# Kernel tuning notes

Hardware: AMD Instinct MI355X
Metric: run time of the kernel (lower is better)

## Reference

```python
import jax, jax.numpy as jnp
import numpy as np

E = 1024      # embed_dim
H = 16        # num_heads
HD = E // H   # head_dim = 64
R = 8         # dora rank
T, B = 2048, 2


def setup_inputs() -> dict:
    key = jax.random.key(0)
    ks = jax.random.split(key, 16)
    query = jax.random.normal(ks[0], (T, B, E), dtype=jnp.float32)
    kk = jax.random.normal(ks[1], (T, B, E), dtype=jnp.float32)
    vv = jax.random.normal(ks[2], (T, B, E), dtype=jnp.float32)

    def make_dora(k1, k2, k3, k4):
        w = jax.random.normal(k1, (E, E), dtype=jnp.float32) * (E ** -0.5)
        m = jnp.linalg.norm(w)            # magnitude scalar (Frobenius norm)
        V = w / m                          # frozen direction, ||V||_F = 1
        A = jax.random.normal(k2, (R, E), dtype=jnp.float32) * (E ** -0.5)
        Bm = jax.random.normal(k3, (E, R), dtype=jnp.float32) * 0.01
        b = jax.random.normal(k4, (E,), dtype=jnp.float32) * 0.01
        return m, V, A, Bm, b

    mag_q, dir_q, A_q, B_q, bias_q = make_dora(ks[3], ks[4], ks[5], ks[6])
    mag_v, dir_v, A_v, B_v, bias_v = make_dora(ks[7], ks[8], ks[9], ks[10])
    k_w = jax.random.normal(ks[11], (E, E), dtype=jnp.float32) * (E ** -0.5)
    k_b = jax.random.normal(ks[12], (E,), dtype=jnp.float32) * 0.01
    out_w = jax.random.normal(ks[13], (E, E), dtype=jnp.float32) * (E ** -0.5)
    out_b = jax.random.normal(ks[14], (E,), dtype=jnp.float32) * 0.01
    return dict(query=query, key=kk, value=vv,
                mag_q=mag_q, dir_q=dir_q, A_q=A_q, B_q=B_q, bias_q=bias_q,
                mag_v=mag_v, dir_v=dir_v, A_v=A_v, B_v=B_v, bias_v=bias_v,
                k_w=k_w, k_b=k_b, out_w=out_w, out_b=out_b)


def _dora_linear(x, m, V, A, Bm, b):
    # W_eff = m * (V + B@A) / (||V + B@A||_F + 1e-8); out = x @ W_eff.T + b
    Vu = V + Bm @ A                      # [E, E]
    W = (m / (jnp.linalg.norm(Vu) + 1e-8)) * Vu
    return x @ W.T + b


def reference(query, key, value, mag_q, dir_q, A_q, B_q, bias_q,
              mag_v, dir_v, A_v, B_v, bias_v, k_w, k_b, out_w, out_b):
    # NOTE: source module ignores `key`/`value` and derives k, v from `query`.
    Tq, Bq, _ = query.shape
    q = _dora_linear(query, mag_q, dir_q, A_q, B_q, bias_q)   # [T, B, E]
    k = query @ k_w.T + k_b                                    # frozen K proj
    v = _dora_linear(query, mag_v, dir_v, A_v, B_v, bias_v)
    # (T, B, E) -> (B*H, T, HD), matching torch reshape/transpose
    q = q.reshape(Tq, Bq * H, HD).transpose(1, 0, 2)
    k = k.reshape(Tq, Bq * H, HD).transpose(1, 0, 2)
    v = v.reshape(Tq, Bq * H, HD).transpose(1, 0, 2)
    scale = HD ** -0.5
    attn = jnp.einsum('nqd,nkd->nqk', q, k) * scale            # [B*H, T, T]
    attn = jax.nn.softmax(attn, axis=-1)                       # dropout p=0
    out = jnp.einsum('nqk,nkd->nqd', attn, v)                  # [B*H, T, HD]
    out = out.transpose(1, 0, 2).reshape(Tq, Bq, E)
    out = out @ out_w.T + out_b
    return out
```

## Files before the change

kernel.cpp:

```cpp
#include <hip/hip_runtime.h>
#include <hip/hip_bf16.h>

#define E_DIM 1024
#define T_DIM 2048
#define B_DIM 2
#define H_DIM 16
#define HD_DIM 64
#define R_DIM 8
#define M_ROWS (T_DIM * B_DIM)
#define LOG2E 1.4426950408889634f

typedef __attribute__((ext_vector_type(8))) short bf16x8;
typedef __attribute__((ext_vector_type(4))) short bf16x4;
typedef __attribute__((ext_vector_type(4))) float f32x4;
typedef __attribute__((ext_vector_type(2))) unsigned uint2v;

#if __has_builtin(__builtin_amdgcn_exp2f)
#define EXP2F(x) __builtin_amdgcn_exp2f(x)
#else
#define EXP2F(x) exp2f(x)
#endif

__device__ __forceinline__ unsigned short f2bf(float f) {
  unsigned int u = __builtin_bit_cast(unsigned int, f);
  u += 0x7FFFu + ((u >> 16) & 1u);
  return (unsigned short)(u >> 16);
}

__device__ __forceinline__ unsigned cvt_pk_bf16(float lo, float hi) {
  unsigned r;
  asm("v_cvt_pk_bf16_f32 %0, %1, %2" : "=v"(r) : "v"(lo), "v"(hi));
  return r;
}

__device__ __forceinline__ f32x4 mfma16(bf16x4 a, bf16x4 b, f32x4 c) {
#if __has_builtin(__builtin_amdgcn_mfma_f32_16x16x16bf16_1k)
  return __builtin_amdgcn_mfma_f32_16x16x16bf16_1k(a, b, c, 0, 0, 0);
#elif __has_builtin(__builtin_amdgcn_mfma_f32_16x16x16_bf16)
  return __builtin_amdgcn_mfma_f32_16x16x16_bf16(a, b, c, 0, 0, 0);
#else
  asm("v_mfma_f32_16x16x16_bf16 %0, %1, %2, %0" : "+v"(c) : "v"(a), "v"(b));
  return c;
#endif
}

__device__ __forceinline__ void glds16(const unsigned short* g, unsigned short* l) {
  __builtin_amdgcn_global_load_lds(
      (__attribute__((address_space(1))) void*)(g),
      (__attribute__((address_space(3))) void*)(l), 16, 0, 0);
}

__global__ __launch_bounds__(256) void prep(
    const float* __restrict__ query, const float* __restrict__ k_w,
    const float* __restrict__ out_w,
    const float* __restrict__ dir_q, const float* __restrict__ A_q, const float* __restrict__ B_q,
    const float* __restrict__ dir_v, const float* __restrict__ A_v, const float* __restrict__ B_v,
    unsigned short* __restrict__ qA_bf, unsigned short* __restrict__ kw_bf,
    unsigned short* __restrict__ ow_bf,
    unsigned short* __restrict__ Wq, unsigned short* __restrict__ Wv,
    float* __restrict__ partials) {
  const int bid = blockIdx.x;
  if (bid < 6144) {
    int u = bid * 256 + threadIdx.x;
    const float* src;
    unsigned short* dst;
    if (u < 1048576) { src = query; dst = qA_bf; }
    else if (u < 1310720) { src = k_w; dst = kw_bf; u -= 1048576; }
    else { src = out_w; dst = ow_bf; u -= 1310720; }
    float4 f = reinterpret_cast<const float4*>(src)[u];
    ushort4 o;
    o.x = f2bf(f.x); o.y = f2bf(f.y); o.z = f2bf(f.z); o.w = f2bf(f.w);
    reinterpret_cast<ushort4*>(dst)[u] = o;
    return;
  }
  const int bid2 = bid - 6144;
  const int mat = bid2 >> 8, bx = bid2 & 255;
  const float* __restrict__ dir = mat ? dir_v : dir_q;
  const float* __restrict__ Am  = mat ? A_v   : A_q;
  const float* __restrict__ Bm  = mat ? B_v   : B_q;
  unsigned short* __restrict__ W = mat ? Wv : Wq;

  float sum = 0.0f;
  for (int idx = bx * 256 + threadIdx.x; idx < E_DIM * E_DIM; idx += 256 * 256) {
    int i = idx >> 10;
    int j = idx & (E_DIM - 1);
    float v = dir[idx];
#pragma unroll
    for (int r = 0; r < R_DIM; ++r)
      v += Bm[i * R_DIM + r] * Am[r * E_DIM + j];
    W[idx] = f2bf(v);
    sum += v * v;
  }
#pragma unroll
  for (int off = 32; off > 0; off >>= 1) sum += __shfl_down(sum, off);
  __shared__ float red[4];
  if ((threadIdx.x & 63) == 0) red[threadIdx.x >> 6] = sum;
  __syncthreads();
  if (threadIdx.x == 0)
    partials[mat * 256 + bx] = (red[0] + red[1]) + (red[2] + red[3]);
}

template <int OUT_MODE>
__device__ __forceinline__ void gemm_bt_core(
    const unsigned short* __restrict__ A, const unsigned short* __restrict__ W,
    const float* __restrict__ bias, float scale, float bscale,
    void* __restrict__ Cptr, int bm, int bn) {
  __shared__ unsigned short As[128 * 32];
  __shared__ unsigned short Bs[128 * 32];
  const int tid = threadIdx.x;
  const int w = tid >> 6, lane = tid & 63;
  const int lr = lane & 15, lg = lane >> 4;
  const int wm = w >> 1, wn = w & 1;

  f32x4 acc[4][4];
#pragma unroll
  for (int i = 0; i < 4; ++i)
#pragma unroll
    for (int j = 0; j < 4; ++j) acc[i][j] = (f32x4){0.f, 0.f, 0.f, 0.f};

  const int c0u = tid, c1u = 256 + tid;
  const int r0 = c0u >> 2, o0 = (c0u & 3) * 8;
  const int r1 = c1u >> 2, o1 = (c1u & 3) * 8;

  for (int k0 = 0; k0 < E_DIM; k0 += 32) {
    glds16(A + (size_t)(bm + r0) * E_DIM + k0 + o0, As + c0u * 8);
    glds16(W + (size_t)(bn + r0) * E_DIM + k0 + o0, Bs + c0u * 8);
    glds16(A + (size_t)(bm + r1) * E_DIM + k0 + o1, As + c1u * 8);
    glds16(W + (size_t)(bn + r1) * E_DIM + k0 + o1, Bs + c1u * 8);
    __syncthreads();

    bf16x8 af[4], bf[4];
#pragma unroll
    for (int i = 0; i < 4; ++i)
      af[i] = *reinterpret_cast<const bf16x8*>(As + (wm * 64 + i * 16 + lr) * 32 + lg * 8);
#pragma unroll
    for (int j = 0; j < 4; ++j)
      bf[j] = *reinterpret_cast<const bf16x8*>(Bs + (wn * 64 + j * 16 + lr) * 32 + lg * 8);
#pragma unroll
    for (int i = 0; i < 4; ++i)
#pragma unroll
      for (int j = 0; j < 4; ++j)
        acc[i][j] = __builtin_amdgcn_mfma_f32_16x16x32_bf16(af[i], bf[j], acc[i][j], 0, 0, 0);
    __syncthreads();
  }

  if (OUT_MODE == 2) {
#pragma unroll
    for (int i = 0; i < 4; ++i) {
      int rowbase = bm + wm * 64 + i * 16 + lg * 4;
      float4 bb = *reinterpret_cast<const float4*>(&bias[rowbase]);
      float bbv[4] = {bb.x, bb.y, bb.z, bb.w};
#pragma unroll
      for (int j = 0; j < 4; ++j) {
        int xrow = bn + wn * 64 + j * 16 + lr;
        int t = xrow >> 1, bsel = xrow & 1;
#pragma unroll
        for (int rr = 0; rr < 4; ++rr) {
          int wrow = rowbase + rr;
          float v = scale * acc[i][j][rr] + bbv[rr];
          int nn = (bsel << 4) | (wrow >> 6);
          int d = wrow & 63;
          reinterpret_cast<unsigned short*>(Cptr)[((size_t)nn * HD_DIM + d) * T_DIM + t] = f2bf(v);
        }
      }
    }
  } else {
#pragma unroll
    for (int i = 0; i < 4; ++i) {
      int row = bm + wm * 64 + i * 16 + lg * 4;
#pragma unroll
      for (int j = 0; j < 4; ++j) {
        int col = bn + wn * 64 + j * 16 + lr;
        float bv = bias[col] * bscale;
#pragma unroll
        for (int r = 0; r < 4; ++r) {
          float v = scale * acc[i][j][r] + bv;
          if (OUT_MODE == 1)
            reinterpret_cast<unsigned short*>(Cptr)[(size_t)(row + r) * E_DIM + col] = f2bf(v);
          else
            reinterpret_cast<float*>(Cptr)[(size_t)(row + r) * E_DIM + col] = v;
        }
      }
    }
  }
}

__global__ __launch_bounds__(256) void gemm_qkv(
    const unsigned short* __restrict__ Abf,
    const unsigned short* __restrict__ Wq, const unsigned short* __restrict__ Wk,
    const unsigned short* __restrict__ Wv,
    const float* __restrict__ bias_q, const float* __restrict__ k_b,
    const float* __restrict__ bias_v,
    const float* __restrict__ partials, const float* __restrict__ mag_q,
    const float* __restrict__ mag_v,
    unsigned short* __restrict__ qbuf, unsigned short* __restrict__ kbuf,
    unsigned short* __restrict__ vT) {
  const int bid = blockIdx.x;
  const int swz = (bid & 7) * 96 + (bid >> 3);
  const int mat = (swz < 256) ? 0 : (swz < 512) ? 1 : 2;

  float scale = 1.0f, bscale = 1.0f;
  if (mat != 1) {
    const int sel = (mat == 0) ? 0 : 1;
    float s = partials[sel * 256 + threadIdx.x];
#pragma unroll
    for (int off = 32; off > 0; off >>= 1) s += __shfl_down(s, off);
    __shared__ float red[4];
    if ((threadIdx.x & 63) == 0) red[threadIdx.x >> 6] = s;
    __syncthreads();
    float tot = (red[0] + red[1]) + (red[2] + red[3]);
    float m = (mat == 0) ? mag_q[0] : mag_v[0];
    float sc = m / (sqrtf(tot) + 1e-8f);
    if (mat == 0) {
      const float sm = 0.125f * LOG2E;
      scale = sc * sm; bscale = sm;
    } else {
      scale = sc;
    }
    __syncthreads();
  }

  if (mat == 0) {
    const int idx = swz;
    gemm_bt_core<1>(Abf, Wq, bias_q, scale, bscale, qbuf,
                    (idx >> 3) * 128, (idx & 7) * 128);
  } else if (mat == 1) {
    const int idx = swz - 256;
    gemm_bt_core<1>(Abf, Wk, k_b, 1.0f, 1.0f, kbuf,
                    (idx >> 3) * 128, (idx & 7) * 128);
  } else {
    const int idx = swz - 512;
    gemm_bt_core<2>(Wv, Abf, bias_v, scale, 1.0f, vT,
                    (idx >> 5) * 128, (idx & 31) * 128);
  }
}

__global__ __launch_bounds__(256) void gemm_out(
    const unsigned short* __restrict__ Abf, const unsigned short* __restrict__ Wo,
    const float* __restrict__ bias, float* __restrict__ out) {
  const int bid = blockIdx.x;
  const int swz = (bid & 7) * 32 + (bid >> 3);
  gemm_bt_core<0>(Abf, Wo, bias, 1.0f, 1.0f, out, (swz >> 3) * 128, (swz & 7) * 128);
}

#define LDPK 72
#define LDPV 136

__global__ __launch_bounds__(512, 2) void attn_mfma(
    const unsigned short* __restrict__ qb, const unsigned short* __restrict__ kb,
    const unsigned short* __restrict__ vT, unsigned short* __restrict__ ob) {
  __shared__ unsigned short Ks2[128 * LDPK];
  __shared__ unsigned short Vt2[64 * LDPV];
  const int n = blockIdx.y, b = n >> 4, col0 = (n & 15) * HD_DIM;
  const int tid = threadIdx.x, w = tid >> 6, lane = tid & 63;
  const int lr = lane & 15, lg = lane >> 4;
  const int q0 = blockIdx.x * 256 + w * 32;

  bf16x8 qf[2][2];
#pragma unroll
  for (int rf = 0; rf < 2; ++rf)
#pragma unroll
    for (int ks = 0; ks < 2; ++ks)
      qf[rf][ks] = *reinterpret_cast<const bf16x8*>(
          qb + ((size_t)(q0 + rf * 16 + lr) * B_DIM + b) * E_DIM + col0 + ks * 32 + lg * 8);

  f32x4 accO[2][4];
#pragma unroll
  for (int rf = 0; rf < 2; ++rf)
#pragma unroll
    for (int df = 0; df < 4; ++df) accO[rf][df] = (f32x4){0.f, 0.f, 0.f, 0.f};
  float mrun0 = -1e30f, mrun1 = -1e30f, lrun0 = 0.f, lrun1 = 0.f;

  const int kr0 = tid >> 3, kc0 = (tid & 7) * 8;
  const int kr1 = 64 + kr0;
  const int vd0 = tid >> 4, vc0 = (tid & 15) * 8;
  const int vd1 = 32 + vd0;
  float4 rk0, rk1, rv0, rv1;
  rk0 = *reinterpret_cast<const float4*>(kb + ((size_t)kr0 * B_DIM + b) * E_DIM + col0 + kc0);
  rk1 = *reinterpret_cast<const float4*>(kb + ((size_t)kr1 * B_DIM + b) * E_DIM + col0 + kc0);
  rv0 = *reinterpret_cast<const float4*>(vT + ((size_t)n * HD_DIM + vd0) * T_DIM + vc0);
  rv1 = *reinterpret_cast<const float4*>(vT + ((size_t)n * HD_DIM + vd1) * T_DIM + vc0);

  for (int kt = 0; kt < T_DIM; kt += 128) {
    __syncthreads();
    *reinterpret_cast<float4*>(Ks2 + kr0 * LDPK + kc0) = rk0;
    *reinterpret_cast<float4*>(Ks2 + kr1 * LDPK + kc0) = rk1;
    *reinterpret_cast<float4*>(Vt2 + vd0 * LDPV + vc0) = rv0;
    *reinterpret_cast<float4*>(Vt2 + vd1 * LDPV + vc0) = rv1;
    __syncthreads();
    if (kt + 128 < T_DIM) {
      int kt2 = kt + 128;
      rk0 = *reinterpret_cast<const float4*>(kb + ((size_t)(kt2 + kr0) * B_DIM + b) * E_DIM + col0 + kc0);
      rk1 = *reinterpret_cast<const float4*>(kb + ((size_t)(kt2 + kr1) * B_DIM + b) * E_DIM + col0 + kc0);
      rv0 = *reinterpret_cast<const float4*>(vT + ((size_t)n * HD_DIM + vd0) * T_DIM + kt2 + vc0);
      rv1 = *reinterpret_cast<const float4*>(vT + ((size_t)n * HD_DIM + vd1) * T_DIM + kt2 + vc0);
    }

#pragma unroll
    for (int h = 0; h < 2; ++h) {
      const unsigned short* Kh = Ks2 + h * 64 * LDPK;
      const unsigned short* Vh = Vt2 + h * 64;

      f32x4 s[4][2];
#pragma unroll
      for (int kf = 0; kf < 4; ++kf)
#pragma unroll
        for (int rf = 0; rf < 2; ++rf) s[kf][rf] = (f32x4){0.f, 0.f, 0.f, 0.f};
      __builtin_amdgcn_s_setprio(1);
#pragma unroll
      for (int ks = 0; ks < 2; ++ks)
#pragma unroll
        for (int kf = 0; kf < 4; ++kf) {
          bf16x8 kfr = *reinterpret_cast<const bf16x8*>(Kh + (kf * 16 + lr) * LDPK + ks * 32 + lg * 8);
#pragma unroll
          for (int rf = 0; rf < 2; ++rf)
            s[kf][rf] = __builtin_amdgcn_mfma_f32_16x16x32_bf16(kfr, qf[rf][ks], s[kf][rf], 0, 0, 0);
        }
      __builtin_amdgcn_s_setprio(0);

      float pm0, pm1;
      {
        float a0 = fmaxf(fmaxf(s[0][0][0], s[0][0][1]), fmaxf(s[0][0][2], s[0][0][3]));
        float a1 = fmaxf(fmaxf(s[1][0][0], s[1][0][1]), fmaxf(s[1][0][2], s[1][0][3]));
        float a2 = fmaxf(fmaxf(s[2][0][0], s[2][0][1]), fmaxf(s[2][0][2], s[2][0][3]));
        float a3 = fmaxf(fmaxf(s[3][0][0], s[3][0][1]), fmaxf(s[3][0][2], s[3][0][3]));
        pm0 = fmaxf(fmaxf(a0, a1), fmaxf(a2, a3));
        float b0 = fmaxf(fmaxf(s[0][1][0], s[0][1][1]), fmaxf(s[0][1][2], s[0][1][3]));
        float b1 = fmaxf(fmaxf(s[1][1][0], s[1][1][1]), fmaxf(s[1][1][2], s[1][1][3]));
        float b2 = fmaxf(fmaxf(s[2][1][0], s[2][1][1]), fmaxf(s[2][1][2], s[2][1][3]));
        float b3 = fmaxf(fmaxf(s[3][1][0], s[3][1][1]), fmaxf(s[3][1][2], s[3][1][3]));
        pm1 = fmaxf(fmaxf(b0, b1), fmaxf(b2, b3));
      }
      pm0 = fmaxf(pm0, __shfl_xor(pm0, 16)); pm0 = fmaxf(pm0, __shfl_xor(pm0, 32));
      pm1 = fmaxf(pm1, __shfl_xor(pm1, 16)); pm1 = fmaxf(pm1, __shfl_xor(pm1, 32));

      const int resc = __any((pm0 > mrun0 + 8.0f) || (pm1 > mrun1 + 8.0f));
      float mn0 = mrun0, mn1 = mrun1;
      if (resc) { mn0 = fmaxf(mn0, pm0); mn1 = fmaxf(mn1, pm1); }

#pragma unroll
      for (int kf = 0; kf < 4; ++kf)
#pragma unroll
        for (int r = 0; r < 4; ++r) {
          s[kf][0][r] = EXP2F(s[kf][0][r] - mn0);
          s[kf][1][r] = EXP2F(s[kf][1][r] - mn1);
        }

      bf16x4 pa4[2][4];
#pragma unroll
      for (int rf = 0; rf < 2; ++rf)
#pragma unroll
        for (int kf = 0; kf < 4; ++kf) {
          uint2v u = (uint2v){cvt_pk_bf16(s[kf][rf][0], s[kf][rf][1]),
                              cvt_pk_bf16(s[kf][rf][2], s[kf][rf][3])};
          pa4[rf][kf] = __builtin_bit_cast(bf16x4, u);
        }

      f32x4 u0 = (s[0][0] + s[1][0]) + (s[2][0] + s[3][0]);
      f32x4 u1 = (s[0][1] + s[1][1]) + (s[2][1] + s[3][1]);
      float ps0 = (u0[0] + u0[1]) + (u0[2] + u0[3]);
      float ps1 = (u1[0] + u1[1]) + (u1[2] + u1[3]);
      ps0 += __shfl_xor(ps0, 16); ps0 += __shfl_xor(ps0, 32);
      ps1 += __shfl_xor(ps1, 16); ps1 += __shfl_xor(ps1, 32);

      if (resc) {
        float al0 = EXP2F(mrun0 - mn0), al1 = EXP2F(mrun1 - mn1);
        mrun0 = mn0; mrun1 = mn1;
        lrun0 = lrun0 * al0 + ps0; lrun1 = lrun1 * al1 + ps1;
#pragma unroll
        for (int r = 0; r < 4; ++r) {
          float a0 = __shfl(al0, (lg << 2) | r);
          float a1 = __shfl(al1, (lg << 2) | r);
#pragma unroll
          for (int df = 0; df < 4; ++df) { accO[0][df][r] *= a0; accO[1][df][r] *= a1; }
        }
      } else {
        lrun0 += ps0; lrun1 += ps1;
      }

      __builtin_amdgcn_s_setprio(1);
#pragma unroll
      for (int kf = 0; kf < 4; ++kf) {
#pragma unroll
        for (int df = 0; df < 4; ++df) {
          bf16x4 vf4 = *reinterpret_cast<const bf16x4*>(
              Vh + (df * 16 + lr) * LDPV + kf * 16 + lg * 4);
          accO[0][df] = mfma16(pa4[0][kf], vf4, accO[0][df]);
          accO[1][df] = mfma16(pa4[1][kf], vf4, accO[1][df]);
        }
      }
      __builtin_amdgcn_s_setprio(0);
    }
  }

#pragma unroll
  for (int rf = 0; rf < 2; ++rf)
#pragma unroll
    for (int r = 0; r < 4; ++r) {
      float lv = __shfl(rf ? lrun1 : lrun0, (lg << 2) | r);
      float inv = 1.0f / lv;
      int row = q0 + rf * 16 + lg * 4 + r;
      size_t base = ((size_t)row * B_DIM + b) * E_DIM + col0;
#pragma unroll
      for (int df = 0; df < 4; ++df)
        ob[base + df * 16 + lr] = f2bf(accO[rf][df][r] * inv);
    }
}

extern "C" void kernel_launch(void* const* d_in, const int* in_sizes, int n_in,
                              void* d_out, int out_size, void* d_ws, size_t ws_size,
                              hipStream_t stream) {
  const float* query  = (const float*)d_in[0];
  const float* mag_q  = (const float*)d_in[3];
  const float* dir_q  = (const float*)d_in[4];
  const float* A_q    = (const float*)d_in[5];
  const float* B_q    = (const float*)d_in[6];
  const float* bias_q = (const float*)d_in[7];
  const float* mag_v  = (const float*)d_in[8];
  const float* dir_v  = (const float*)d_in[9];
  const float* A_v    = (const float*)d_in[10];
  const float* B_v    = (const float*)d_in[11];
  const float* bias_v = (const float*)d_in[12];
  const float* k_w    = (const float*)d_in[13];
  const float* k_b    = (const float*)d_in[14];
  const float* out_w  = (const float*)d_in[15];
  const float* out_b  = (const float*)d_in[16];
  float* out = (float*)d_out;

  char* ws = (char*)d_ws;
  float* partials = (float*)ws;
  unsigned short* qA_bf = (unsigned short*)(ws + 4096);
  unsigned short* wq_bf = qA_bf + (size_t)M_ROWS * E_DIM;
  unsigned short* wv_bf = wq_bf + (size_t)E_DIM * E_DIM;
  unsigned short* kw_bf = wv_bf + (size_t)E_DIM * E_DIM;
  unsigned short* ow_bf = kw_bf + (size_t)E_DIM * E_DIM;
  unsigned short* qbuf  = ow_bf + (size_t)E_DIM * E_DIM;
  unsigned short* kbuf  = qbuf + (size_t)M_ROWS * E_DIM;
  unsigned short* vTbuf = kbuf + (size_t)M_ROWS * E_DIM;
  unsigned short* abuf  = vTbuf + (size_t)M_ROWS * E_DIM;

  prep<<<6656, 256, 0, stream>>>(query, k_w, out_w,
                                 dir_q, A_q, B_q, dir_v, A_v, B_v,
                                 qA_bf, kw_bf, ow_bf, wq_bf, wv_bf, partials);

  gemm_qkv<<<768, 256, 0, stream>>>(qA_bf, wq_bf, kw_bf, wv_bf,
                                    bias_q, k_b, bias_v,
                                    partials, mag_q, mag_v,
                                    qbuf, kbuf, vTbuf);
  attn_mfma<<<dim3(T_DIM / 256, B_DIM * H_DIM), 512, 0, stream>>>(
      qbuf, kbuf, vTbuf, abuf);
  gemm_out<<<256, 256, 0, stream>>>(abuf, ow_bf, out_b, out);
}
```

Before: 154.6 us.

## Specialize output GEMM kernel and swap attention grid axes for head-major scheduling

The output projection no longer calls the shared GEMM core. It gets its own kernel that stages bf16 A and B tiles in shared memory with register prefetch of the next K slice, runs 16x16x32 MFMAs, and writes fp32 output plus bias directly. The shared core's fp32 output branch is removed, so that core now only emits bf16. The attention grid is transposed so consecutive blocks walk heads first, which changes how blocks map to K/V data and may change L2 reuse. The hand-written GEMM may not match the tuned core's scheduling and adds duplicated code.

```diff
diff --git a/kernel.cpp b/kernel.cpp
--- a/kernel.cpp
+++ b/kernel.cpp
@@ -175,10 +175,7 @@
 #pragma unroll
         for (int r = 0; r < 4; ++r) {
           float v = scale * acc[i][j][r] + bv;
-          if (OUT_MODE == 1)
-            reinterpret_cast<unsigned short*>(Cptr)[(size_t)(row + r) * E_DIM + col] = f2bf(v);
-          else
-            reinterpret_cast<float*>(Cptr)[(size_t)(row + r) * E_DIM + col] = v;
+          reinterpret_cast<unsigned short*>(Cptr)[(size_t)(row + r) * E_DIM + col] = f2bf(v);
         }
       }
     }
@@ -240,7 +237,71 @@
     const float* __restrict__ bias, float* __restrict__ out) {
   const int bid = blockIdx.x;
   const int swz = (bid & 7) * 32 + (bid >> 3);
-  gemm_bt_core<0>(Abf, Wo, bias, 1.0f, 1.0f, out, (swz >> 3) * 128, (swz & 7) * 128);
+  const int bm = (swz >> 3) * 128, bn = (swz & 7) * 128;
+
+  __shared__ unsigned short As[128 * 32];
+  __shared__ unsigned short Bs[128 * 32];
+  const int tid = threadIdx.x;
+  const int w = tid >> 6, lane = tid & 63;
+  const int lr = lane & 15, lg = lane >> 4;
+  const int wm = w >> 1, wn = w & 1;
+
+  f32x4 acc[4][4];
+#pragma unroll
+  for (int i = 0; i < 4; ++i)
+#pragma unroll
+    for (int j = 0; j < 4; ++j) acc[i][j] = (f32x4){0.f, 0.f, 0.f, 0.f};
+
+  const int c0u = tid, c1u = 256 + tid;
+  const int r0 = c0u >> 2, o0 = (c0u & 3) * 8;
+  const int r1 = c1u >> 2, o1 = (c1u & 3) * 8;
+
+  float4 ra0, ra1, rb0, rb1;
+  ra0 = *reinterpret_cast<const float4*>(Abf + (size_t)(bm + r0) * E_DIM + o0);
+  ra1 = *reinterpret_cast<const float4*>(Abf + (size_t)(bm + r1) * E_DIM + o1);
+  rb0 = *reinterpret_cast<const float4*>(Wo + (size_t)(bn + r0) * E_DIM + o0);
+  rb1 = *reinterpret_cast<const float4*>(Wo + (size_t)(bn + r1) * E_DIM + o1);
+
+  for (int k0 = 0; k0 < E_DIM; k0 += 32) {
+    __syncthreads();
+    *reinterpret_cast<float4*>(As + c0u * 8) = ra0;
+    *reinterpret_cast<float4*>(As + c1u * 8) = ra1;
+    *reinterpret_cast<float4*>(Bs + c0u * 8) = rb0;
+    *reinterpret_cast<float4*>(Bs + c1u * 8) = rb1;
+    __syncthreads();
+    if (k0 + 32 < E_DIM) {
+      ra0 = *reinterpret_cast<const float4*>(Abf + (size_t)(bm + r0) * E_DIM + k0 + 32 + o0);
+      ra1 = *reinterpret_cast<const float4*>(Abf + (size_t)(bm + r1) * E_DIM + k0 + 32 + o1);
+      rb0 = *reinterpret_cast<const float4*>(Wo + (size_t)(bn + r0) * E_DIM + k0 + 32 + o0);
+      rb1 = *reinterpret_cast<const float4*>(Wo + (size_t)(bn + r1) * E_DIM + k0 + 32 + o1);
+    }
+
+    bf16x8 af[4], bf[4];
+#pragma unroll
+    for (int i = 0; i < 4; ++i)
+      af[i] = *reinterpret_cast<const bf16x8*>(As + (wm * 64 + i * 16 + lr) * 32 + lg * 8);
+#pragma unroll
+    for (int j = 0; j < 4; ++j)
+      bf[j] = *reinterpret_cast<const bf16x8*>(Bs + (wn * 64 + j * 16 + lr) * 32 + lg * 8);
+#pragma unroll
+    for (int i = 0; i < 4; ++i)
+#pragma unroll
+      for (int j = 0; j < 4; ++j)
+        acc[i][j] = __builtin_amdgcn_mfma_f32_16x16x32_bf16(af[i], bf[j], acc[i][j], 0, 0, 0);
+  }
+
+#pragma unroll
+  for (int i = 0; i < 4; ++i) {
+    int row = bm + wm * 64 + i * 16 + lg * 4;
+#pragma unroll
+    for (int j = 0; j < 4; ++j) {
+      int col = bn + wn * 64 + j * 16 + lr;
+      float bv = bias[col];
+#pragma unroll
+      for (int r = 0; r < 4; ++r)
+        out[(size_t)(row + r) * E_DIM + col] = acc[i][j][r] + bv;
+    }
+  }
 }
 
 #define LDPK 72
@@ -251,10 +312,10 @@
     const unsigned short* __restrict__ vT, unsigned short* __restrict__ ob) {
   __shared__ unsigned short Ks2[128 * LDPK];
   __shared__ unsigned short Vt2[64 * LDPV];
-  const int n = blockIdx.y, b = n >> 4, col0 = (n & 15) * HD_DIM;
+  const int n = blockIdx.x, b = n >> 4, col0 = (n & 15) * HD_DIM;
   const int tid = threadIdx.x, w = tid >> 6, lane = tid & 63;
   const int lr = lane & 15, lg = lane >> 4;
-  const int q0 = blockIdx.x * 256 + w * 32;
+  const int q0 = blockIdx.y * 256 + w * 32;
 
   bf16x8 qf[2][2];
 #pragma unroll
@@ -447,7 +508,7 @@
                                     bias_q, k_b, bias_v,
                                     partials, mag_q, mag_v,
                                     qbuf, kbuf, vTbuf);
-  attn_mfma<<<dim3(T_DIM / 256, B_DIM * H_DIM), 512, 0, stream>>>(
+  attn_mfma<<<dim3(B_DIM * H_DIM, T_DIM / 256), 512, 0, stream>>>(
       qbuf, kbuf, vTbuf, abuf);
   gemm_out<<<256, 256, 0, stream>>>(abuf, ow_bf, out_b, out);
 }
```

Result: no change. 153.3 us (-0.8%).
